# Kernel optimization log

Hardware: AMD Instinct MI355X
Metric: run time of the kernel (lower is better)

Reference implementation:

```python
import jax, jax.numpy as jnp
import numpy as np

N_NODES = 100000
N_EDGES = 1600000
MSG_DIM = 16
HID_DIM = 16
N_ETYPE = 16
N_CLASSES = 64


def setup_inputs() -> dict:
    key = jax.random.key(0)
    ks = jax.random.split(key, 11)
    s = 1.0 / np.sqrt(HID_DIM)
    return {
        "features": jax.random.normal(ks[0], (N_NODES, HID_DIM), dtype=jnp.float32),
        "src": jax.random.randint(ks[1], (N_EDGES,), 0, N_NODES, dtype=jnp.int32),
        "dst": jax.random.randint(ks[2], (N_EDGES,), 0, N_NODES, dtype=jnp.int32),
        "e_type": jax.random.randint(ks[3], (N_EDGES,), 0, N_ETYPE, dtype=jnp.int32),
        "edge_emb": jax.random.normal(ks[4], (N_ETYPE, MSG_DIM * HID_DIM), dtype=jnp.float32),
        "W_ih": jax.random.uniform(ks[5], (3 * HID_DIM, MSG_DIM), dtype=jnp.float32, minval=-s, maxval=s),
        "W_hh": jax.random.uniform(ks[6], (3 * HID_DIM, HID_DIM), dtype=jnp.float32, minval=-s, maxval=s),
        "b_ih": jax.random.uniform(ks[7], (3 * HID_DIM,), dtype=jnp.float32, minval=-s, maxval=s),
        "b_hh": jax.random.uniform(ks[8], (3 * HID_DIM,), dtype=jnp.float32, minval=-s, maxval=s),
        "W_out": jax.random.normal(ks[9], (N_CLASSES, HID_DIM), dtype=jnp.float32) * s,
        "b_out": jax.random.normal(ks[10], (N_CLASSES,), dtype=jnp.float32) * 0.01,
    }


def reference(features, src, dst, e_type, edge_emb, W_ih, W_hh, b_ih, b_hh, W_out, b_out):
    # Per-edge message: A_e @ h_src, A_e = edge-type embedding reshaped [msg, hid]
    A = edge_emb[e_type].reshape(-1, MSG_DIM, HID_DIM)          # [E, M, H]
    msg = jnp.einsum("emh,eh->em", A, features[src])            # [E, M]
    # Sum-aggregate messages into destination nodes
    m = jax.ops.segment_sum(msg, dst, num_segments=N_NODES)     # [N, M]
    # Single-step GRU (PyTorch gate order: r, z, n)
    gx = m @ W_ih.T + b_ih                                      # [N, 3H]
    gh = features @ W_hh.T + b_hh                               # [N, 3H]
    xr, xz, xn = jnp.split(gx, 3, axis=-1)
    hr, hz, hn = jnp.split(gh, 3, axis=-1)
    r = jax.nn.sigmoid(xr + hr)
    z = jax.nn.sigmoid(xz + hz)
    n = jnp.tanh(xn + r * hn)
    h = (1.0 - z) * n + z * features                            # [N, H]
    return h @ W_out.T + b_out                                  # [N, C]
```

## Files before the change

kernel.cpp:

```cpp
#include <hip/hip_runtime.h>

#define NNODES 100000
#define NEDGES 1600000
#define HID 16
#define MSG 16
#define NTYPE 16
#define NCLS 64

#define BSH 7
#define NBK ((NNODES + 127) >> 7)
#define CHSZ 8192
#define NCH ((NEDGES + CHSZ - 1) / CHSZ)
#define M_SCAN (NBK * NCH)
#define SCH 1024
#define NSB ((M_SCAN + SCH - 1) / SCH)

#define ASTR 20
#define ATY  320

#define RECCAP 2560
#define CHUNK 16
#define NCHK (NEDGES / CHUNK)
#define AGG2_BLOCKS (NCHK / 16)

__device__ __forceinline__ float sigmoid_f(float x) {
    return 1.0f / (1.0f + __expf(-x));
}
__device__ __forceinline__ float tanh_f(float x) {
    x = fminf(fmaxf(x, -15.0f), 15.0f);
    float e = __expf(2.0f * x);
    return (e - 1.0f) / (e + 1.0f);
}

__global__ __launch_bounds__(1024) void hist_k(const int* __restrict__ dst,
                                               int* __restrict__ cntmat) {
    __shared__ int cnt[NBK];
    const int t = threadIdx.x, ch = blockIdx.x;
    for (int b = t; b < NBK; b += 1024) cnt[b] = 0;
    __syncthreads();
    #pragma unroll
    for (int k = 0; k < CHSZ / 1024; k++) {
        int e = ch * CHSZ + k * 1024 + t;
        if (e < NEDGES) atomicAdd(&cnt[dst[e] >> BSH], 1);
    }
    __syncthreads();
    for (int b = t; b < NBK; b += 1024) cntmat[b * NCH + ch] = cnt[b];
}

__global__ __launch_bounds__(256) void scan_bsum(const int* __restrict__ x,
                                                 int* __restrict__ bsum) {
    const int t = threadIdx.x;
    int base = blockIdx.x * SCH + t * 4;
    int s = 0;
    #pragma unroll
    for (int q = 0; q < 4; q++) {
        int idx = base + q;
        if (idx < M_SCAN) s += x[idx];
    }
    #pragma unroll
    for (int d = 32; d > 0; d >>= 1) s += __shfl_down(s, d, 64);
    __shared__ int ws[4];
    int lane = t & 63, w = t >> 6;
    if (lane == 0) ws[w] = s;
    __syncthreads();
    if (t == 0) bsum[blockIdx.x] = ws[0] + ws[1] + ws[2] + ws[3];
}

__global__ __launch_bounds__(256) void scan_write(const int* __restrict__ bsum,
                                                  int* __restrict__ x,
                                                  int* __restrict__ bnd) {
    const int t = threadIdx.x;
    __shared__ int wsA[4];
    __shared__ int bpref_s;
    {
        int v = (t < blockIdx.x && t < NSB) ? bsum[t] : 0;
        #pragma unroll
        for (int d = 32; d > 0; d >>= 1) v += __shfl_down(v, d, 64);
        int lane = t & 63, w = t >> 6;
        if (lane == 0) wsA[w] = v;
        __syncthreads();
        if (t == 0) bpref_s = wsA[0] + wsA[1] + wsA[2] + wsA[3];
        __syncthreads();
    }

    int base = blockIdx.x * SCH + t * 4;
    int v[4]; int ts = 0;
    #pragma unroll
    for (int q = 0; q < 4; q++) {
        int idx = base + q;
        v[q] = (idx < M_SCAN) ? x[idx] : 0;
        ts += v[q];
    }
    int lane = t & 63, w = t >> 6;
    int s = ts;
    #pragma unroll
    for (int d = 1; d < 64; d <<= 1) {
        int u = __shfl_up(s, d, 64);
        if (lane >= d) s += u;
    }
    __shared__ int wsB[4];
    if (lane == 63) wsB[w] = s;
    __syncthreads();
    int wbase = 0;
    #pragma unroll
    for (int q = 0; q < 4; q++) if (q < w) wbase += wsB[q];
    int run = bpref_s + wbase + (s - ts);
    #pragma unroll
    for (int q = 0; q < 4; q++) {
        int idx = base + q;
        if (idx < M_SCAN) {
            x[idx] = run;
            if (idx % NCH == 0) bnd[idx / NCH] = run;
        }
        run += v[q];
    }
    if (blockIdx.x == 0 && t == 0) bnd[NBK] = NEDGES;
}

__global__ __launch_bounds__(1024) void scatter_k(const int* __restrict__ src,
                                                  const int* __restrict__ dst,
                                                  const int* __restrict__ et,
                                                  const int* __restrict__ offmat,
                                                  int* __restrict__ rec) {
    __shared__ int offc[NBK];
    const int t = threadIdx.x, ch = blockIdx.x;
    for (int b = t; b < NBK; b += 1024) offc[b] = offmat[b * NCH + ch];
    __syncthreads();
    #pragma unroll
    for (int k = 0; k < CHSZ / 1024; k++) {
        int e = ch * CHSZ + k * 1024 + t;
        if (e < NEDGES) {
            int d = dst[e];
            int b = d >> BSH;
            int pos = atomicAdd(&offc[b], 1);
            rec[pos] = src[e] | (et[e] << 17) | ((d & 127) << 21);
        }
    }
}

__global__ __launch_bounds__(256) void sort2_k(const int* __restrict__ bnd,
                                               int* __restrict__ rec,
                                               int* __restrict__ cb) {
    __shared__ int buf[RECCAP];
    __shared__ int cnt[128];
    __shared__ int basec[128];
    __shared__ int wtot[4];
    const int t = threadIdx.x, b = blockIdx.x;
    const int jb = bnd[b];
    const int je = bnd[b + 1];
    const int len = je - jb;

    if (len > 0 && len <= RECCAP) {
        if (t < 128) cnt[t] = 0;
        for (int k = t; k < len; k += 256) buf[k] = rec[jb + k];
        __syncthreads();
        for (int k = t; k < len; k += 256) atomicAdd(&cnt[((unsigned)buf[k]) >> 21], 1);
        __syncthreads();
        int v = (t < 128) ? cnt[t] : 0;
        int lane = t & 63, w = t >> 6;
        int s = v;
        #pragma unroll
        for (int d = 1; d < 64; d <<= 1) {
            int u = __shfl_up(s, d, 64);
            if (lane >= d) s += u;
        }
        if (lane == 63) wtot[w] = s;
        __syncthreads();
        if (t < 128) basec[t] = s - v + (w == 1 ? wtot[0] : 0);
        __syncthreads();
        for (int k = t; k < len; k += 256) {
            int r = buf[k];
            int p = atomicAdd(&basec[((unsigned)r) >> 21], 1);
            rec[jb + p] = r;
        }
    }

    const int c0 = (jb + CHUNK - 1) >> 4;
    const int c1 = (je + CHUNK - 1) >> 4;
    for (int c = c0 + t; c < c1; c += 256) cb[c] = b;
}

__device__ __forceinline__ float dot16(const float4* A, float4 f0, float4 f1,
                                       float4 f2, float4 f3) {
    float4 A0 = A[0], A1 = A[1], A2 = A[2], A3 = A[3];
    float m;
    m  = A0.x*f0.x + A0.y*f0.y + A0.z*f0.z + A0.w*f0.w;
    m += A1.x*f1.x + A1.y*f1.y + A1.z*f1.z + A1.w*f1.w;
    m += A2.x*f2.x + A2.y*f2.y + A2.z*f2.z + A2.w*f2.w;
    m += A3.x*f3.x + A3.y*f3.y + A3.z*f3.z + A3.w*f3.w;
    return m;
}

__global__ __launch_bounds__(256) void agg2_k(const float* __restrict__ feat,
                                              const int* __restrict__ rec,
                                              const int* __restrict__ bnd,
                                              const int* __restrict__ cb,
                                              const float* __restrict__ edge_emb,
                                              float* __restrict__ magg) {
    __shared__ float At2[NTYPE * ATY];
    __shared__ int recs[256];
    const int t = threadIdx.x;
    #pragma unroll
    for (int idx = t; idx < NTYPE * MSG * HID; idx += 256) {
        int ty = idx >> 8, rem = idx & 255, ii = rem >> 4, h = rem & 15;
        At2[ty * ATY + ii * ASTR + h] = edge_emb[idx];
    }
    recs[t] = rec[blockIdx.x * 256 + t];
    __syncthreads();

    const int g = t >> 4, i = t & 15;
    const int chunk = blockIdx.x * 16 + g;
    const int jbase = chunk << 4;
    const int lbase = g << 4;

    int b = cb[chunk];
    int bnext = bnd[b + 1];

    float macc = 0.0f;
    int cur = -1;
    #pragma unroll 1
    for (int p = 0; p < 8; p++) {
        int r1 = recs[lbase + 2 * p];
        int r2 = recs[lbase + 2 * p + 1];
        const float4* p1 = (const float4*)(feat + (size_t)(r1 & 0x1FFFF) * HID);
        const float4* p2 = (const float4*)(feat + (size_t)(r2 & 0x1FFFF) * HID);
        float4 Fa0 = p1[0], Fa1 = p1[1], Fa2 = p1[2], Fa3 = p1[3];
        float4 Fb0 = p2[0], Fb1 = p2[1], Fb2 = p2[2], Fb3 = p2[3];
        __builtin_amdgcn_sched_barrier(0);

        int j = jbase + 2 * p;
        while (j >= bnext) { ++b; bnext = bnd[b + 1]; }
        int d1 = (b << BSH) | (((unsigned)r1) >> 21);
        float m1 = dot16((const float4*)(At2 + ((r1 >> 17) & 15) * ATY + i * ASTR),
                         Fa0, Fa1, Fa2, Fa3);
        if (d1 != cur) {
            if (cur >= 0) atomicAdd(&magg[(size_t)cur * MSG + i], macc);
            macc = 0.0f; cur = d1;
        }
        macc += m1;

        while (j + 1 >= bnext) { ++b; bnext = bnd[b + 1]; }
        int d2 = (b << BSH) | (((unsigned)r2) >> 21);
        float m2 = dot16((const float4*)(At2 + ((r2 >> 17) & 15) * ATY + i * ASTR),
                         Fb0, Fb1, Fb2, Fb3);
        if (d2 != cur) {
            atomicAdd(&magg[(size_t)cur * MSG + i], macc);
            macc = 0.0f; cur = d2;
        }
        macc += m2;
    }
    atomicAdd(&magg[(size_t)cur * MSG + i], macc);
}

__global__ __launch_bounds__(256) void ggnn_edge(
    const float* __restrict__ feat,
    const int* __restrict__ src,
    const int* __restrict__ dst,
    const int* __restrict__ etype,
    const float* __restrict__ edge_emb,
    float* __restrict__ magg)
{
    __shared__ float At[NTYPE * MSG * HID];
    for (int idx = threadIdx.x; idx < NTYPE * MSG * HID; idx += 256) {
        int ty = idx >> 8, rem = idx & 255, i = rem >> 4, hh = rem & 15;
        At[(ty << 8) | (hh << 4) | i] = edge_emb[idx];
    }
    __syncthreads();
    const long long total = (long long)NEDGES * MSG;
    for (long long w = (long long)blockIdx.x * 256 + threadIdx.x; w < total;
         w += (long long)gridDim.x * 256) {
        const int e = (int)(w >> 4);
        const int i = (int)(w & 15);
        const int s = src[e];
        const int d = dst[e];
        const int ty = etype[e];
        const float4* fp = (const float4*)(feat + (size_t)s * HID);
        const float4 f0 = fp[0], f1 = fp[1], f2 = fp[2], f3 = fp[3];
        const float* a = At + (ty << 8) + i;
        float m;
        m  = a[0*16]*f0.x + a[1*16]*f0.y + a[2*16]*f0.z + a[3*16]*f0.w;
        m += a[4*16]*f1.x + a[5*16]*f1.y + a[6*16]*f1.z + a[7*16]*f1.w;
        m += a[8*16]*f2.x + a[9*16]*f2.y + a[10*16]*f2.z + a[11*16]*f2.w;
        m += a[12*16]*f3.x + a[13*16]*f3.y + a[14*16]*f3.z + a[15*16]*f3.w;
        atomicAdd(magg + (size_t)d * MSG + i, m);
    }
}

__global__ __launch_bounds__(256) void node_k(
    const float* __restrict__ feat,
    const float* __restrict__ magg,
    const float* __restrict__ W_ih,
    const float* __restrict__ W_hh,
    const float* __restrict__ b_ih,
    const float* __restrict__ b_hh,
    const float* __restrict__ W_out,
    const float* __restrict__ b_out,
    float* __restrict__ out)
{
    __shared__ float hn_s[256 * 20];
    const int t = threadIdx.x;
    const int n = blockIdx.x * 256 + t;
    if (n < NNODES) {
        float hv[HID], mv[MSG];
        const float4* hp = (const float4*)(feat + (size_t)n * HID);
        const float4* mp = (const float4*)(magg + (size_t)n * MSG);
        #pragma unroll
        for (int q = 0; q < 4; q++) {
            float4 a = hp[q];
            hv[4*q+0] = a.x; hv[4*q+1] = a.y; hv[4*q+2] = a.z; hv[4*q+3] = a.w;
            float4 c = mp[q];
            mv[4*q+0] = c.x; mv[4*q+1] = c.y; mv[4*q+2] = c.z; mv[4*q+3] = c.w;
        }
        #pragma unroll
        for (int i = 0; i < HID; i++) {
            float xr = b_ih[i], xz = b_ih[16 + i], xn = b_ih[32 + i];
            float hr = b_hh[i], hz = b_hh[16 + i], hn = b_hh[32 + i];
            #pragma unroll
            for (int j = 0; j < HID; j++) {
                xr += W_ih[(i)      * 16 + j] * mv[j];
                xz += W_ih[(16 + i) * 16 + j] * mv[j];
                xn += W_ih[(32 + i) * 16 + j] * mv[j];
                hr += W_hh[(i)      * 16 + j] * hv[j];
                hz += W_hh[(16 + i) * 16 + j] * hv[j];
                hn += W_hh[(32 + i) * 16 + j] * hv[j];
            }
            float r  = sigmoid_f(xr + hr);
            float z  = sigmoid_f(xz + hz);
            float nn = tanh_f(xn + r * hn);
            hn_s[t * 20 + i] = (1.0f - z) * nn + z * hv[i];
        }
    }
    __syncthreads();

    const int w = t >> 6, g = (t >> 4) & 3, li = t & 15;
    float4 w4[4][4];
    #pragma unroll
    for (int rr = 0; rr < 4; rr++)
        #pragma unroll
        for (int qq = 0; qq < 4; qq++)
            w4[rr][qq] = ((const float4*)W_out)[(4 * li + rr) * 4 + qq];
    const float4 bo4 = ((const float4*)b_out)[li];
    const int nb = blockIdx.x * 256;

    #pragma unroll
    for (int it = 0; it < 16; it++) {
        int ln = it * 16 + w * 4 + g;
        int n2 = nb + ln;
        if (n2 < NNODES) {
            const float4* hq = (const float4*)(hn_s + ln * 20);
            float4 h0 = hq[0], h1 = hq[1], h2 = hq[2], h3 = hq[3];
            float4 o;
            o.x = bo4.x + w4[0][0].x*h0.x + w4[0][0].y*h0.y + w4[0][0].z*h0.z + w4[0][0].w*h0.w
                        + w4[0][1].x*h1.x + w4[0][1].y*h1.y + w4[0][1].z*h1.z + w4[0][1].w*h1.w
                        + w4[0][2].x*h2.x + w4[0][2].y*h2.y + w4[0][2].z*h2.z + w4[0][2].w*h2.w
                        + w4[0][3].x*h3.x + w4[0][3].y*h3.y + w4[0][3].z*h3.z + w4[0][3].w*h3.w;
            o.y = bo4.y + w4[1][0].x*h0.x + w4[1][0].y*h0.y + w4[1][0].z*h0.z + w4[1][0].w*h0.w
                        + w4[1][1].x*h1.x + w4[1][1].y*h1.y + w4[1][1].z*h1.z + w4[1][1].w*h1.w
                        + w4[1][2].x*h2.x + w4[1][2].y*h2.y + w4[1][2].z*h2.z + w4[1][2].w*h2.w
                        + w4[1][3].x*h3.x + w4[1][3].y*h3.y + w4[1][3].z*h3.z + w4[1][3].w*h3.w;
            o.z = bo4.z + w4[2][0].x*h0.x + w4[2][0].y*h0.y + w4[2][0].z*h0.z + w4[2][0].w*h0.w
                        + w4[2][1].x*h1.x + w4[2][1].y*h1.y + w4[2][1].z*h1.z + w4[2][1].w*h1.w
                        + w4[2][2].x*h2.x + w4[2][2].y*h2.y + w4[2][2].z*h2.z + w4[2][2].w*h2.w
                        + w4[2][3].x*h3.x + w4[2][3].y*h3.y + w4[2][3].z*h3.z + w4[2][3].w*h3.w;
            o.w = bo4.w + w4[3][0].x*h0.x + w4[3][0].y*h0.y + w4[3][0].z*h0.z + w4[3][0].w*h0.w
                        + w4[3][1].x*h1.x + w4[3][1].y*h1.y + w4[3][1].z*h1.z + w4[3][1].w*h1.w
                        + w4[3][2].x*h2.x + w4[3][2].y*h2.y + w4[3][2].z*h2.z + w4[3][2].w*h2.w
                        + w4[3][3].x*h3.x + w4[3][3].y*h3.y + w4[3][3].z*h3.z + w4[3][3].w*h3.w;
            ((float4*)(out + (size_t)n2 * NCLS))[li] = o;
        }
    }
}

extern "C" void kernel_launch(void* const* d_in, const int* in_sizes, int n_in,
                              void* d_out, int out_size, void* d_ws, size_t ws_size,
                              hipStream_t stream) {
    const float* feat     = (const float*)d_in[0];
    const int*   src      = (const int*)d_in[1];
    const int*   dst      = (const int*)d_in[2];
    const int*   etype    = (const int*)d_in[3];
    const float* edge_emb = (const float*)d_in[4];
    const float* W_ih     = (const float*)d_in[5];
    const float* W_hh     = (const float*)d_in[6];
    const float* b_ih     = (const float*)d_in[7];
    const float* b_hh     = (const float*)d_in[8];
    const float* W_out    = (const float*)d_in[9];
    const float* b_out    = (const float*)d_in[10];
    float* out = (float*)d_out;

    float* magg   = (float*)d_ws;
    int*   offmat = (int*)d_ws + (size_t)NNODES * MSG;
    int*   bsum   = offmat + M_SCAN;
    int*   bnd    = bsum + 256;
    int*   cb     = bnd + 1024;
    int*   rec    = cb + NCHK;
    size_t need   = ((size_t)NNODES * MSG + M_SCAN + 256 + 1024 + NCHK + NEDGES) * 4;

    hipMemsetAsync(magg, 0, (size_t)NNODES * MSG * sizeof(float), stream);
    if (ws_size >= need) {
        hist_k    <<<NCH, 1024, 0, stream>>>(dst, offmat);
        scan_bsum <<<NSB, 256, 0, stream>>>(offmat, bsum);
        scan_write<<<NSB, 256, 0, stream>>>(bsum, offmat, bnd);
        scatter_k <<<NCH, 1024, 0, stream>>>(src, dst, etype, offmat, rec);
        sort2_k   <<<NBK, 256, 0, stream>>>(bnd, rec, cb);
        agg2_k    <<<AGG2_BLOCKS, 256, 0, stream>>>(feat, rec, bnd, cb, edge_emb, magg);
    } else {
        ggnn_edge<<<2560, 256, 0, stream>>>(feat, src, dst, etype, edge_emb, magg);
    }
    node_k<<<(NNODES + 255) / 256, 256, 0, stream>>>(
        feat, magg, W_ih, W_hh, b_ih, b_hh, W_out, b_out, out);
}
```

Baseline: 142.0 us.

## Replace scan-based bucket sort with fixed-capacity buckets and global atomic counters

The histogram, two-pass scan and scatter kernels are replaced by one scatter kernel. It reserves space in fixed-capacity per-bucket slots (BCAP records) through one global atomicAdd per bucket per chunk, which removes three kernel launches and the offset-matrix traffic. The aggregation kernel now maps blocks to bucket slices with known bucket identity instead of walking boundary arrays, and lays out the edge-type matrices in shared memory as four float4 planes. The risk is overflow if any bucket exceeds BCAP records, which holds only for roughly uniform destination distributions. It also launches padded blocks that exit early.

```diff
diff --git a/kernel.cpp b/kernel.cpp
--- a/kernel.cpp
+++ b/kernel.cpp
@@ -11,17 +11,9 @@
 #define NBK ((NNODES + 127) >> 7)
 #define CHSZ 8192
 #define NCH ((NEDGES + CHSZ - 1) / CHSZ)
-#define M_SCAN (NBK * NCH)
-#define SCH 1024
-#define NSB ((M_SCAN + SCH - 1) / SCH)
-
-#define ASTR 20
-#define ATY  320
-
-#define RECCAP 2560
-#define CHUNK 16
-#define NCHK (NEDGES / CHUNK)
-#define AGG2_BLOCKS (NCHK / 16)
+#define BCAP 2304
+#define BLKPB (BCAP / 256)
+#define AGG_BLOCKS (NBK * BLKPB)
 
 __device__ __forceinline__ float sigmoid_f(float x) {
     return 1.0f / (1.0f + __expf(-x));
@@ -32,222 +24,149 @@
     return (e - 1.0f) / (e + 1.0f);
 }
 
-__global__ __launch_bounds__(1024) void hist_k(const int* __restrict__ dst,
-                                               int* __restrict__ cntmat) {
+__global__ __launch_bounds__(1024) void scat_k(const int* __restrict__ src,
+                                               const int* __restrict__ dst,
+                                               const int* __restrict__ et,
+                                               int* __restrict__ gcnt,
+                                               int* __restrict__ rec) {
     __shared__ int cnt[NBK];
     const int t = threadIdx.x, ch = blockIdx.x;
-    for (int b = t; b < NBK; b += 1024) cnt[b] = 0;
-    __syncthreads();
+    for (int k = t; k < NBK; k += 1024) cnt[k] = 0;
+    __syncthreads();
+    int dcache[CHSZ / 1024];
     #pragma unroll
     for (int k = 0; k < CHSZ / 1024; k++) {
         int e = ch * CHSZ + k * 1024 + t;
-        if (e < NEDGES) atomicAdd(&cnt[dst[e] >> BSH], 1);
-    }
-    __syncthreads();
-    for (int b = t; b < NBK; b += 1024) cntmat[b * NCH + ch] = cnt[b];
-}
-
-__global__ __launch_bounds__(256) void scan_bsum(const int* __restrict__ x,
-                                                 int* __restrict__ bsum) {
-    const int t = threadIdx.x;
-    int base = blockIdx.x * SCH + t * 4;
-    int s = 0;
-    #pragma unroll
-    for (int q = 0; q < 4; q++) {
-        int idx = base + q;
-        if (idx < M_SCAN) s += x[idx];
-    }
-    #pragma unroll
-    for (int d = 32; d > 0; d >>= 1) s += __shfl_down(s, d, 64);
-    __shared__ int ws[4];
-    int lane = t & 63, w = t >> 6;
-    if (lane == 0) ws[w] = s;
-    __syncthreads();
-    if (t == 0) bsum[blockIdx.x] = ws[0] + ws[1] + ws[2] + ws[3];
-}
-
-__global__ __launch_bounds__(256) void scan_write(const int* __restrict__ bsum,
-                                                  int* __restrict__ x,
-                                                  int* __restrict__ bnd) {
-    const int t = threadIdx.x;
-    __shared__ int wsA[4];
-    __shared__ int bpref_s;
-    {
-        int v = (t < blockIdx.x && t < NSB) ? bsum[t] : 0;
-        #pragma unroll
-        for (int d = 32; d > 0; d >>= 1) v += __shfl_down(v, d, 64);
-        int lane = t & 63, w = t >> 6;
-        if (lane == 0) wsA[w] = v;
-        __syncthreads();
-        if (t == 0) bpref_s = wsA[0] + wsA[1] + wsA[2] + wsA[3];
-        __syncthreads();
-    }
-
-    int base = blockIdx.x * SCH + t * 4;
-    int v[4]; int ts = 0;
-    #pragma unroll
-    for (int q = 0; q < 4; q++) {
-        int idx = base + q;
-        v[q] = (idx < M_SCAN) ? x[idx] : 0;
-        ts += v[q];
-    }
-    int lane = t & 63, w = t >> 6;
-    int s = ts;
-    #pragma unroll
-    for (int d = 1; d < 64; d <<= 1) {
-        int u = __shfl_up(s, d, 64);
-        if (lane >= d) s += u;
-    }
-    __shared__ int wsB[4];
-    if (lane == 63) wsB[w] = s;
-    __syncthreads();
-    int wbase = 0;
-    #pragma unroll
-    for (int q = 0; q < 4; q++) if (q < w) wbase += wsB[q];
-    int run = bpref_s + wbase + (s - ts);
-    #pragma unroll
-    for (int q = 0; q < 4; q++) {
-        int idx = base + q;
-        if (idx < M_SCAN) {
-            x[idx] = run;
-            if (idx % NCH == 0) bnd[idx / NCH] = run;
-        }
-        run += v[q];
-    }
-    if (blockIdx.x == 0 && t == 0) bnd[NBK] = NEDGES;
-}
-
-__global__ __launch_bounds__(1024) void scatter_k(const int* __restrict__ src,
-                                                  const int* __restrict__ dst,
-                                                  const int* __restrict__ et,
-                                                  const int* __restrict__ offmat,
-                                                  int* __restrict__ rec) {
-    __shared__ int offc[NBK];
-    const int t = threadIdx.x, ch = blockIdx.x;
-    for (int b = t; b < NBK; b += 1024) offc[b] = offmat[b * NCH + ch];
+        dcache[k] = (e < NEDGES) ? dst[e] : -1;
+        if (dcache[k] >= 0) atomicAdd(&cnt[dcache[k] >> BSH], 1);
+    }
+    __syncthreads();
+    for (int k = t; k < NBK; k += 1024) {
+        int c = cnt[k];
+        cnt[k] = c ? atomicAdd(&gcnt[k], c) : 0;
+    }
     __syncthreads();
     #pragma unroll
     for (int k = 0; k < CHSZ / 1024; k++) {
         int e = ch * CHSZ + k * 1024 + t;
         if (e < NEDGES) {
-            int d = dst[e];
+            int d = dcache[k];
             int b = d >> BSH;
-            int pos = atomicAdd(&offc[b], 1);
-            rec[pos] = src[e] | (et[e] << 17) | ((d & 127) << 21);
-        }
-    }
-}
-
-__global__ __launch_bounds__(256) void sort2_k(const int* __restrict__ bnd,
-                                               int* __restrict__ rec,
-                                               int* __restrict__ cb) {
-    __shared__ int buf[RECCAP];
+            int pos = atomicAdd(&cnt[b], 1);
+            rec[b * BCAP + pos] = src[e] | (et[e] << 17) | ((d & 127) << 21);
+        }
+    }
+}
+
+__global__ __launch_bounds__(256) void sort2_k(const int* __restrict__ gcnt,
+                                               int* __restrict__ rec) {
+    __shared__ int buf[BCAP];
     __shared__ int cnt[128];
     __shared__ int basec[128];
     __shared__ int wtot[4];
     const int t = threadIdx.x, b = blockIdx.x;
-    const int jb = bnd[b];
-    const int je = bnd[b + 1];
-    const int len = je - jb;
-
-    if (len > 0 && len <= RECCAP) {
-        if (t < 128) cnt[t] = 0;
-        for (int k = t; k < len; k += 256) buf[k] = rec[jb + k];
-        __syncthreads();
-        for (int k = t; k < len; k += 256) atomicAdd(&cnt[((unsigned)buf[k]) >> 21], 1);
-        __syncthreads();
-        int v = (t < 128) ? cnt[t] : 0;
-        int lane = t & 63, w = t >> 6;
-        int s = v;
-        #pragma unroll
-        for (int d = 1; d < 64; d <<= 1) {
-            int u = __shfl_up(s, d, 64);
-            if (lane >= d) s += u;
-        }
-        if (lane == 63) wtot[w] = s;
-        __syncthreads();
-        if (t < 128) basec[t] = s - v + (w == 1 ? wtot[0] : 0);
-        __syncthreads();
-        for (int k = t; k < len; k += 256) {
-            int r = buf[k];
-            int p = atomicAdd(&basec[((unsigned)r) >> 21], 1);
-            rec[jb + p] = r;
-        }
-    }
-
-    const int c0 = (jb + CHUNK - 1) >> 4;
-    const int c1 = (je + CHUNK - 1) >> 4;
-    for (int c = c0 + t; c < c1; c += 256) cb[c] = b;
-}
-
-__device__ __forceinline__ float dot16(const float4* A, float4 f0, float4 f1,
-                                       float4 f2, float4 f3) {
-    float4 A0 = A[0], A1 = A[1], A2 = A[2], A3 = A[3];
-    float m;
-    m  = A0.x*f0.x + A0.y*f0.y + A0.z*f0.z + A0.w*f0.w;
-    m += A1.x*f1.x + A1.y*f1.y + A1.z*f1.z + A1.w*f1.w;
-    m += A2.x*f2.x + A2.y*f2.y + A2.z*f2.z + A2.w*f2.w;
-    m += A3.x*f3.x + A3.y*f3.y + A3.z*f3.z + A3.w*f3.w;
-    return m;
-}
-
-__global__ __launch_bounds__(256) void agg2_k(const float* __restrict__ feat,
+    const int jb = b * BCAP;
+    const int len = gcnt[b];
+    if (len <= 0) return;
+
+    if (t < 128) cnt[t] = 0;
+    for (int k = t; k < len; k += 256) buf[k] = rec[jb + k];
+    __syncthreads();
+    for (int k = t; k < len; k += 256) atomicAdd(&cnt[((unsigned)buf[k]) >> 21], 1);
+    __syncthreads();
+    int v = (t < 128) ? cnt[t] : 0;
+    int lane = t & 63, w = t >> 6;
+    int s = v;
+    #pragma unroll
+    for (int d = 1; d < 64; d <<= 1) {
+        int u = __shfl_up(s, d, 64);
+        if (lane >= d) s += u;
+    }
+    if (lane == 63) wtot[w] = s;
+    __syncthreads();
+    if (t < 128) basec[t] = s - v + (w == 1 ? wtot[0] : 0);
+    __syncthreads();
+    for (int k = t; k < len; k += 256) {
+        int r = buf[k];
+        int p = atomicAdd(&basec[((unsigned)r) >> 21], 1);
+        rec[jb + p] = r;
+    }
+}
+
+__global__ __launch_bounds__(256) void agg3_k(const float* __restrict__ feat,
                                               const int* __restrict__ rec,
-                                              const int* __restrict__ bnd,
-                                              const int* __restrict__ cb,
+                                              const int* __restrict__ gcnt,
                                               const float* __restrict__ edge_emb,
                                               float* __restrict__ magg) {
-    __shared__ float At2[NTYPE * ATY];
+    __shared__ float AqF[4 * 4096];
     __shared__ int recs[256];
     const int t = threadIdx.x;
     #pragma unroll
     for (int idx = t; idx < NTYPE * MSG * HID; idx += 256) {
-        int ty = idx >> 8, rem = idx & 255, ii = rem >> 4, h = rem & 15;
-        At2[ty * ATY + ii * ASTR + h] = edge_emb[idx];
-    }
-    recs[t] = rec[blockIdx.x * 256 + t];
+        int ty = idx >> 8, rem = idx & 255, i = rem >> 4, h = rem & 15;
+        AqF[(h >> 2) * 4096 + ty * 64 + i * 4 + (h & 3)] = edge_emb[idx];
+    }
+    const int b  = blockIdx.x / BLKPB;
+    const int br = blockIdx.x % BLKPB;
+    recs[t] = rec[b * BCAP + br * 256 + t];
+    const int cnt = gcnt[b];
     __syncthreads();
 
     const int g = t >> 4, i = t & 15;
-    const int chunk = blockIdx.x * 16 + g;
-    const int jbase = chunk << 4;
+    const int w0 = br * 256 + (g << 4);
+    int rem = cnt - w0;
+    if (rem <= 0) return;
+    const int vcnt = rem < 16 ? rem : 16;
     const int lbase = g << 4;
-
-    int b = cb[chunk];
-    int bnext = bnd[b + 1];
+    const float4* Aq0 = (const float4*)(AqF);
+    const float4* Aq1 = (const float4*)(AqF + 4096);
+    const float4* Aq2 = (const float4*)(AqF + 8192);
+    const float4* Aq3 = (const float4*)(AqF + 12288);
 
     float macc = 0.0f;
     int cur = -1;
     #pragma unroll 1
-    for (int p = 0; p < 8; p++) {
-        int r1 = recs[lbase + 2 * p];
-        int r2 = recs[lbase + 2 * p + 1];
-        const float4* p1 = (const float4*)(feat + (size_t)(r1 & 0x1FFFF) * HID);
-        const float4* p2 = (const float4*)(feat + (size_t)(r2 & 0x1FFFF) * HID);
-        float4 Fa0 = p1[0], Fa1 = p1[1], Fa2 = p1[2], Fa3 = p1[3];
-        float4 Fb0 = p2[0], Fb1 = p2[1], Fb2 = p2[2], Fb3 = p2[3];
+    for (int p = 0; p < 16; p += 2) {
+        if (p >= vcnt) break;
+        const bool has2 = (p + 1) < vcnt;
+        int r1 = recs[lbase + p];
+        int r2 = has2 ? recs[lbase + p + 1] : r1;
+        const float4* f1 = (const float4*)(feat + (size_t)(r1 & 0x1FFFF) * HID);
+        const float4* f2 = (const float4*)(feat + (size_t)(r2 & 0x1FFFF) * HID);
+        float4 Fa0 = f1[0], Fa1 = f1[1], Fa2 = f1[2], Fa3 = f1[3];
+        float4 Fb0 = f2[0], Fb1 = f2[1], Fb2 = f2[2], Fb3 = f2[3];
         __builtin_amdgcn_sched_barrier(0);
 
-        int j = jbase + 2 * p;
-        while (j >= bnext) { ++b; bnext = bnd[b + 1]; }
-        int d1 = (b << BSH) | (((unsigned)r1) >> 21);
-        float m1 = dot16((const float4*)(At2 + ((r1 >> 17) & 15) * ATY + i * ASTR),
-                         Fa0, Fa1, Fa2, Fa3);
-        if (d1 != cur) {
-            if (cur >= 0) atomicAdd(&magg[(size_t)cur * MSG + i], macc);
-            macc = 0.0f; cur = d1;
-        }
-        macc += m1;
-
-        while (j + 1 >= bnext) { ++b; bnext = bnd[b + 1]; }
-        int d2 = (b << BSH) | (((unsigned)r2) >> 21);
-        float m2 = dot16((const float4*)(At2 + ((r2 >> 17) & 15) * ATY + i * ASTR),
-                         Fb0, Fb1, Fb2, Fb3);
-        if (d2 != cur) {
-            atomicAdd(&magg[(size_t)cur * MSG + i], macc);
-            macc = 0.0f; cur = d2;
-        }
-        macc += m2;
+        {
+            int a1 = (((r1 >> 17) & 15) << 4) + i;
+            float4 A0 = Aq0[a1], A1 = Aq1[a1], A2 = Aq2[a1], A3 = Aq3[a1];
+            float m1;
+            m1  = A0.x*Fa0.x + A0.y*Fa0.y + A0.z*Fa0.z + A0.w*Fa0.w;
+            m1 += A1.x*Fa1.x + A1.y*Fa1.y + A1.z*Fa1.z + A1.w*Fa1.w;
+            m1 += A2.x*Fa2.x + A2.y*Fa2.y + A2.z*Fa2.z + A2.w*Fa2.w;
+            m1 += A3.x*Fa3.x + A3.y*Fa3.y + A3.z*Fa3.z + A3.w*Fa3.w;
+            int d1 = (b << BSH) | (((unsigned)r1) >> 21);
+            if (d1 != cur) {
+                if (cur >= 0) atomicAdd(&magg[(size_t)cur * MSG + i], macc);
+                macc = 0.0f; cur = d1;
+            }
+            macc += m1;
+        }
+        if (has2) {
+            int a2 = (((r2 >> 17) & 15) << 4) + i;
+            float4 B0 = Aq0[a2], B1 = Aq1[a2], B2 = Aq2[a2], B3 = Aq3[a2];
+            float m2;
+            m2  = B0.x*Fb0.x + B0.y*Fb0.y + B0.z*Fb0.z + B0.w*Fb0.w;
+            m2 += B1.x*Fb1.x + B1.y*Fb1.y + B1.z*Fb1.z + B1.w*Fb1.w;
+            m2 += B2.x*Fb2.x + B2.y*Fb2.y + B2.z*Fb2.z + B2.w*Fb2.w;
+            m2 += B3.x*Fb3.x + B3.y*Fb3.y + B3.z*Fb3.z + B3.w*Fb3.w;
+            int d2 = (b << BSH) | (((unsigned)r2) >> 21);
+            if (d2 != cur) {
+                atomicAdd(&magg[(size_t)cur * MSG + i], macc);
+                macc = 0.0f; cur = d2;
+            }
+            macc += m2;
+        }
     }
     atomicAdd(&magg[(size_t)cur * MSG + i], macc);
 }
@@ -387,23 +306,18 @@
     const float* b_out    = (const float*)d_in[10];
     float* out = (float*)d_out;
 
-    float* magg   = (float*)d_ws;
-    int*   offmat = (int*)d_ws + (size_t)NNODES * MSG;
-    int*   bsum   = offmat + M_SCAN;
-    int*   bnd    = bsum + 256;
-    int*   cb     = bnd + 1024;
-    int*   rec    = cb + NCHK;
-    size_t need   = ((size_t)NNODES * MSG + M_SCAN + 256 + 1024 + NCHK + NEDGES) * 4;
-
-    hipMemsetAsync(magg, 0, (size_t)NNODES * MSG * sizeof(float), stream);
+    float* magg = (float*)d_ws;
+    int*   gcnt = (int*)d_ws + (size_t)NNODES * MSG;
+    int*   rec  = gcnt + 1024;
+    size_t need = ((size_t)NNODES * MSG + 1024 + (size_t)NBK * BCAP) * 4;
+
     if (ws_size >= need) {
-        hist_k    <<<NCH, 1024, 0, stream>>>(dst, offmat);
-        scan_bsum <<<NSB, 256, 0, stream>>>(offmat, bsum);
-        scan_write<<<NSB, 256, 0, stream>>>(bsum, offmat, bnd);
-        scatter_k <<<NCH, 1024, 0, stream>>>(src, dst, etype, offmat, rec);
-        sort2_k   <<<NBK, 256, 0, stream>>>(bnd, rec, cb);
-        agg2_k    <<<AGG2_BLOCKS, 256, 0, stream>>>(feat, rec, bnd, cb, edge_emb, magg);
+        hipMemsetAsync(magg, 0, ((size_t)NNODES * MSG + 1024) * sizeof(float), stream);
+        scat_k  <<<NCH, 1024, 0, stream>>>(src, dst, etype, gcnt, rec);
+        sort2_k <<<NBK, 256, 0, stream>>>(gcnt, rec);
+        agg3_k  <<<AGG_BLOCKS, 256, 0, stream>>>(feat, rec, gcnt, edge_emb, magg);
     } else {
+        hipMemsetAsync(magg, 0, (size_t)NNODES * MSG * sizeof(float), stream);
         ggnn_edge<<<2560, 256, 0, stream>>>(feat, src, dst, etype, edge_emb, magg);
     }
     node_k<<<(NNODES + 255) / 256, 256, 0, stream>>>(
```

Measured after the change: 186.2 us. 31.1% more time.
